# Kernel tuning notes

Hardware: AMD Instinct MI355X
Metric: run time of the kernel (lower is better)

## Reference

```python
import jax, jax.numpy as jnp
import numpy as np

EPS = 1e-7        # min norm to avoid div-by-zero
BALL_EPS = 1e-5   # Poincare-ball boundary clip


def _norm(x):
    return jnp.maximum(jnp.linalg.norm(x, axis=-1, keepdims=True), EPS)


def expmap0(u, c):
    sc = jnp.sqrt(c)
    n = _norm(u)
    return jnp.tanh(sc * n) * u / (sc * n)


def logmap0(p, c):
    sc = jnp.sqrt(c)
    n = _norm(p)
    return jnp.arctanh(jnp.minimum(sc * n, 1.0 - BALL_EPS)) * p / (sc * n)


def proj(x, c):
    # project onto the ball of radius (1-eps)/sqrt(c)
    n = _norm(x)
    maxn = (1.0 - BALL_EPS) / jnp.sqrt(c)
    return jnp.where(n > maxn, x * (maxn / n), x)


def mobius_matvec(W, x, c):
    # Mobius matrix-vector multiply on the Poincare ball
    sc = jnp.sqrt(c)
    xn = _norm(x)                       # [N,1]
    mx = x @ W                          # [N,D]
    mxn = _norm(mx)
    t = jnp.tanh((mxn / xn) * jnp.arctanh(jnp.minimum(sc * xn, 1.0 - BALL_EPS)))
    return t * mx / (sc * mxn)


def spmm(rows, cols, vals, x):
    # sparse(adj) @ x, adjacency in COO form
    return jax.ops.segment_sum(vals[:, None] * x[cols], rows, num_segments=x.shape[0])


def hgc_layer(x, rows, cols, vals, W, c, c_lin):
    t = logmap0(x, c)                               # to tangent space at origin
    h = proj(mobius_matvec(W, t, c_lin), c_lin)     # LinearHyperbolic (c=1.0, no activation)
    s = spmm(rows, cols, vals, h)                   # HyperbolicAggregation: adj @ h
    agg = proj(expmap0(s, c), c)
    a = jax.nn.relu(logmap0(agg, c))                # ActivationHyperbolic (relu, c_in=c_out=c)
    return proj(expmap0(a, c), c)


def setup_inputs() -> dict:
    key = jax.random.key(0)
    ks = jax.random.split(key, 7)
    N, D, E = 10000, 1433, 100000
    x = jax.random.normal(ks[0], (N, D), jnp.float32) * 0.1  # keep points off the boundary
    rows = jax.random.randint(ks[1], (E,), 0, N)
    cols = jax.random.randint(ks[2], (E,), 0, N)
    vals = jax.random.uniform(ks[3], (E,), jnp.float32) / 10.0  # ~normalized adjacency weights
    scale = 1.0 / np.sqrt(D)
    W0 = jax.random.normal(ks[4], (D, D), jnp.float32) * scale
    W1 = jax.random.normal(ks[5], (D, D), jnp.float32) * scale
    W2 = jax.random.normal(ks[6], (D, D), jnp.float32) * scale
    return {"x": x, "W0": W0, "W1": W1, "W2": W2, "vals": vals, "rows": rows, "cols": cols}


def reference(x, W0, W1, W2, vals, rows, cols):
    c = jnp.float32(0.4)       # c_map == c0 for every layer in the source
    c_lin = jnp.float32(1.0)   # LinearHyperbolic hard-coded c
    h = expmap0(x, c)
    for W in (W0, W1, W2):
        h = hgc_layer(h, rows, cols, vals, W, c, c_lin)
    return h
```

## Files before the change

kernel.cpp:

```cpp
#include <hip/hip_runtime.h>

typedef unsigned short u16;
typedef unsigned int   u32;

#define M_ROWS 10000
#define D_DIM  1433
#define KPAD   1536
#define MPAD   10240
#define N_EDGE 100000
#define HPAD   1440
#define HP32   720
#define NKT    24
#define EPS    1e-7f
#define BEPS   1e-5f
#define SC     0.6324555320336759f

typedef __bf16 bf16x8 __attribute__((ext_vector_type(8)));
typedef float  f32x4  __attribute__((ext_vector_type(4)));
typedef u32    u32x4  __attribute__((ext_vector_type(4)));

__device__ __forceinline__ u16 f2bf(float f) {
  union { float f; unsigned u; } v; v.f = f;
  unsigned r = v.u + 0x7FFFu + ((v.u >> 16) & 1u);
  return (u16)(r >> 16);
}
__device__ __forceinline__ u32 pack2bf(float lo, float hi) {
  return (u32)f2bf(lo) | ((u32)f2bf(hi) << 16);
}
__device__ __forceinline__ float bflo(u32 u) { return __uint_as_float(u << 16); }
__device__ __forceinline__ float bfhi(u32 u) { return __uint_as_float(u & 0xFFFF0000u); }

__device__ __forceinline__ float atanh_f(float y) {
  return 0.5f * logf((1.f + y) / (1.f - y));
}

__device__ __forceinline__ void gl_lds16(const u16* g, u16* l) {
  __builtin_amdgcn_global_load_lds((const __attribute__((address_space(1))) void*)(const void*)g,
                                   (__attribute__((address_space(3))) void*)(void*)l,
                                   16, 0, 0);
}

__global__ __launch_bounds__(512, 1) void gemm256(
    const u16* __restrict__ A,
    const u16* __restrict__ B,
    u16* __restrict__ C,
    float* __restrict__ nrm)
{
  __shared__ u16 lds[2][2][256 * 64];

  const int tid  = threadIdx.x;
  const int lane = tid & 63;
  const int w    = tid >> 6;
  const int wr   = w >> 2;
  const int wc   = w & 3;

  const int flat = blockIdx.x;
  const int wgid = (flat & 7) * 30 + (flat >> 3);
  const int gy = wgid % 6;
  const int gx = wgid / 6;
  const long arow0 = (long)gx * 256;
  const long brow0 = (long)gy * 256;

  f32x4 acc[8][4] = {};

  const int sr8 = lane >> 3;
  const int scb = ((lane & 7) << 4) ^ (sr8 << 4);

  auto STAGE = [&](int b, int kt) {
    const long k0 = (long)kt * 64 + (scb >> 1);
#pragma unroll
    for (int l = 0; l < 4; ++l) {
      const int r   = l * 64 + w * 8 + sr8;
      const int dst = l * 4096 + w * 512;
      gl_lds16(A + (arow0 + r) * KPAD + k0, &lds[b][0][dst]);
      gl_lds16(B + (brow0 + r) * KPAD + k0, &lds[b][1][dst]);
    }
  };

  STAGE(0, 0);
  __syncthreads();

  for (int kt = 0; kt < NKT; ++kt) {
    const int b = kt & 1;
    if (kt < NKT - 1) STAGE(b ^ 1, kt + 1);
#pragma unroll
    for (int ks = 0; ks < 2; ++ks) {
      bf16x8 af[8], bfr[4];
#pragma unroll
      for (int mi = 0; mi < 8; ++mi) {
        const int row = wr * 128 + mi * 16 + (lane & 15);
        const int kb  = (ks * 64 + ((lane >> 4) << 4)) ^ ((row & 7) << 4);
        af[mi] = *(const bf16x8*)&lds[b][0][row * 64 + (kb >> 1)];
      }
#pragma unroll
      for (int ni = 0; ni < 4; ++ni) {
        const int row = wc * 64 + ni * 16 + (lane & 15);
        const int kb  = (ks * 64 + ((lane >> 4) << 4)) ^ ((row & 7) << 4);
        bfr[ni] = *(const bf16x8*)&lds[b][1][row * 64 + (kb >> 1)];
      }
#pragma unroll
      for (int mi = 0; mi < 8; ++mi)
#pragma unroll
        for (int ni = 0; ni < 4; ++ni)
          acc[mi][ni] = __builtin_amdgcn_mfma_f32_16x16x32_bf16(af[mi], bfr[ni], acc[mi][ni], 0, 0, 0);
    }
    __syncthreads();
  }

  const int orw = (lane >> 4) * 4;
  const int ocl = lane & 15;

#pragma unroll
  for (int mi = 0; mi < 8; ++mi)
#pragma unroll
    for (int r = 0; r < 4; ++r) {
      float s = 0.f;
#pragma unroll
      for (int ni = 0; ni < 4; ++ni) {
        const long j = brow0 + wc * 64 + ni * 16 + ocl;
        const float v = acc[mi][ni][r];
        s += (j < D_DIM) ? v * v : 0.f;
      }
      s += __shfl_xor(s, 1, 64);
      s += __shfl_xor(s, 2, 64);
      s += __shfl_xor(s, 4, 64);
      s += __shfl_xor(s, 8, 64);
      if ((lane & 15) == 0)
        atomicAdd(&nrm[arow0 + wr * 128 + mi * 16 + orw + r], s);
    }

#pragma unroll
  for (int mi = 0; mi < 8; ++mi) {
    const long i0 = arow0 + wr * 128 + mi * 16 + orw;
    if (i0 >= M_ROWS) continue;
#pragma unroll
    for (int ni = 0; ni < 4; ++ni) {
      const long j = brow0 + wc * 64 + ni * 16 + ocl;
      if (j >= HPAD) continue;
#pragma unroll
      for (int r = 0; r < 4; ++r) {
        const long i = i0 + r;
        if (i < M_ROWS) C[i * HPAD + j] = (j < D_DIM) ? f2bf(acc[mi][ni][r]) : (u16)0;
      }
    }
  }
}

__device__ __forceinline__ float2 block_reduce2(float a, float b) {
  __shared__ float sa[4], sb[4];
#pragma unroll
  for (int off = 32; off > 0; off >>= 1) {
    a += __shfl_down(a, off, 64);
    b += __shfl_down(b, off, 64);
  }
  const int tid = threadIdx.x;
  if ((tid & 63) == 0) { sa[tid >> 6] = a; sb[tid >> 6] = b; }
  __syncthreads();
  const float ra = sa[0] + sa[1] + sa[2] + sa[3];
  const float rb = sb[0] + sb[1] + sb[2] + sb[3];
  __syncthreads();
  return make_float2(ra, rb);
}

__global__ __launch_bounds__(256) void pre_k(const float* __restrict__ x,
                                             u16* __restrict__ t,
                                             float* __restrict__ xn) {
  const long i = blockIdx.x;
  const int tid = threadIdx.x;
  u16* trow = t + i * KPAD;
  if (i >= M_ROWS) {
#pragma unroll
    for (int jj = 0; jj < 6; ++jj) { int j = tid + jj * 256; if (j < KPAD) trow[j] = 0; }
    return;
  }
  const float* xr = x + i * D_DIM;
  float v[6]; float s2 = 0.f;
#pragma unroll
  for (int jj = 0; jj < 6; ++jj) {
    int j = tid + jj * 256;
    v[jj] = (j < D_DIM) ? xr[j] : 0.f;
    s2 += v[jj] * v[jj];
  }
  s2 = block_reduce2(s2, 0.f).x;
  const float nx_t = sqrtf(s2);
  const float nx   = fmaxf(nx_t, EPS);
  const float al   = tanhf(SC * nx) / (SC * nx);
  const float n1   = fmaxf(al * nx_t, EPS);
  const float be   = atanh_f(fminf(SC * n1, 1.f - BEPS)) / (SC * n1);
  const float sca  = al * be;
  if (tid == 0) xn[i] = fmaxf(sca * nx_t, EPS);
#pragma unroll
  for (int jj = 0; jj < 6; ++jj) {
    int j = tid + jj * 256;
    if (j < KPAD) trow[j] = (j < D_DIM) ? f2bf(sca * v[jj]) : (u16)0;
  }
}

__global__ void zero_f(float* p, int n) {
  int i = blockIdx.x * 256 + threadIdx.x;
  if (i < n) p[i] = 0.f;
}

__global__ void fold_k(const int* __restrict__ ecol, const float* __restrict__ eval,
                       const float* __restrict__ nrm, const float* __restrict__ xn,
                       u32* __restrict__ pe, int E) {
  const int e = blockIdx.x * 256 + threadIdx.x;
  if (e >= E) return;
  const int c = ecol[e];
  const float realn = sqrtf(nrm[c]);
  const float mxn   = fmaxf(realn, EPS);
  const float xi    = xn[c];
  const float tf    = tanhf((mxn / xi) * atanh_f(fminf(xi, 1.f - BEPS)));
  float S = tf / mxn;
  const float hn = fmaxf(S * realn, EPS);
  const float maxn = 1.f - BEPS;
  if (hn > maxn) S *= maxn / hn;
  pe[e] = ((u32)c << 16) | (u32)f2bf(eval[e] * S);
}

__global__ __launch_bounds__(256) void spmm_post(const int* __restrict__ rp,
                                                 const u32* __restrict__ pe,
                                                 const u32* __restrict__ mxp,
                                                 u16* __restrict__ t,
                                                 float* __restrict__ xn,
                                                 float* __restrict__ out,
                                                 const int last) {
  const long r = blockIdx.x;
  const int tid = threadIdx.x;
  if (r >= M_ROWS) {
    if (!last && tid < 192) {
      u32* trow32 = (u32*)(t + r * KPAD);
#pragma unroll
      for (int k = 0; k < 4; ++k) trow32[4 * tid + k] = 0u;
    }
    return;
  }
  const bool act = tid < 180;
  const long boff = 4 * tid;
  float a[8] = {0.f, 0.f, 0.f, 0.f, 0.f, 0.f, 0.f, 0.f};
  const int e0 = rp[r], e1 = rp[r + 1];
  int e = e0;
  for (; e + 7 < e1; e += 8) {
    u32 pp[8];
#pragma unroll
    for (int j = 0; j < 8; ++j) pp[j] = pe[e + j];
    if (act) {
      u32x4 q[8];
#pragma unroll
      for (int j = 0; j < 8; ++j)
        q[j] = *(const u32x4*)&mxp[(long)(pp[j] >> 16) * HP32 + boff];
#pragma unroll
      for (int j = 0; j < 8; ++j) {
        const float w = bflo(pp[j]);
#pragma unroll
        for (int k = 0; k < 4; ++k) {
          a[2 * k]     += w * bflo(q[j][k]);
          a[2 * k + 1] += w * bfhi(q[j][k]);
        }
      }
    }
  }
  for (; e + 3 < e1; e += 4) {
    u32 pp[4];
#pragma unroll
    for (int j = 0; j < 4; ++j) pp[j] = pe[e + j];
    if (act) {
      u32x4 q[4];
#pragma unroll
      for (int j = 0; j < 4; ++j)
        q[j] = *(const u32x4*)&mxp[(long)(pp[j] >> 16) * HP32 + boff];
#pragma unroll
      for (int j = 0; j < 4; ++j) {
        const float w = bflo(pp[j]);
#pragma unroll
        for (int k = 0; k < 4; ++k) {
          a[2 * k]     += w * bflo(q[j][k]);
          a[2 * k + 1] += w * bfhi(q[j][k]);
        }
      }
    }
  }
  for (; e < e1; ++e) {
    const u32 p0 = pe[e];
    if (act) {
      const u32x4 q0 = *(const u32x4*)&mxp[(long)(p0 >> 16) * HP32 + boff];
      const float w0 = bflo(p0);
#pragma unroll
      for (int k = 0; k < 4; ++k) {
        a[2 * k]     += w0 * bflo(q0[k]);
        a[2 * k + 1] += w0 * bfhi(q0[k]);
      }
    }
  }
  float s2 = 0.f, s2p = 0.f;
#pragma unroll
  for (int k = 0; k < 8; ++k) {
    const int col = 8 * tid + k;
    const float v = (act && col < D_DIM) ? a[k] : 0.f;
    a[k] = v;
    s2 += v * v;
    const float p = fmaxf(v, 0.f);
    s2p += p * p;
  }
  const float2 red = block_reduce2(s2, s2p);
  const float ns_t  = sqrtf(red.x);
  const float nsp_t = sqrtf(red.y);
  const float maxn = (1.f - BEPS) / SC;
  const float ns = fmaxf(ns_t, EPS);
  const float al = tanhf(SC * ns) / (SC * ns);
  const float n1 = fmaxf(al * ns_t, EPS);
  const float be = (n1 > maxn) ? (maxn / n1) : 1.f;
  const float n2 = fmaxf(be * al * ns_t, EPS);
  const float lam = atanh_f(fminf(SC * n2, 1.f - BEPS)) / (SC * n2);
  const float g = lam * be * al;
  const float na_t = g * nsp_t;
  const float n3 = fmaxf(na_t, EPS);
  const float mu = tanhf(SC * n3) / (SC * n3);
  const float n4 = fmaxf(mu * na_t, EPS);
  const float nu = (n4 > maxn) ? (maxn / n4) : 1.f;
  const float T = nu * mu * g;
  if (last) {
    if (act) {
      float* orow = out + r * (long)D_DIM;
#pragma unroll
      for (int k = 0; k < 8; ++k) {
        const int col = 8 * tid + k;
        if (col < D_DIM) orow[col] = T * fmaxf(a[k], 0.f);
      }
    }
  } else {
    const float nh_t = T * nsp_t;
    const float n5 = fmaxf(nh_t, EPS);
    const float kap = atanh_f(fminf(SC * n5, 1.f - BEPS)) / (SC * n5);
    const float F = kap * T;
    if (tid == 0) xn[r] = fmaxf(F * nsp_t, EPS);
    u32* trow32 = (u32*)(t + r * KPAD);
    if (act) {
#pragma unroll
      for (int k = 0; k < 4; ++k)
        trow32[4 * tid + k] = pack2bf(F * fmaxf(a[2 * k], 0.f), F * fmaxf(a[2 * k + 1], 0.f));
    } else if (tid < 192) {
#pragma unroll
      for (int k = 0; k < 4; ++k) trow32[4 * tid + k] = 0u;
    }
  }
}

__global__ void wt_conv(const float* __restrict__ W, u16* __restrict__ Wt) {
  __shared__ float tile[32][33];
  const int kb = blockIdx.x * 32, nb = blockIdx.y * 32;
  const int tx = threadIdx.x, ty = threadIdx.y;
#pragma unroll
  for (int r = 0; r < 32; r += 8) {
    const int k = kb + ty + r, n = nb + tx;
    tile[ty + r][tx] = (k < D_DIM && n < D_DIM) ? W[(long)k * D_DIM + n] : 0.f;
  }
  __syncthreads();
#pragma unroll
  for (int r = 0; r < 32; r += 8) {
    const int n = nb + ty + r, k = kb + tx;
    if (n < KPAD && k < KPAD) Wt[(long)n * KPAD + k] = f2bf(tile[tx][ty + r]);
  }
}

__global__ void zero_int(int* p, int n) {
  int i = blockIdx.x * 256 + threadIdx.x;
  if (i < n) p[i] = 0;
}
__global__ void hist_k(const int* __restrict__ rows, int* __restrict__ counts, int E) {
  int e = blockIdx.x * 256 + threadIdx.x;
  if (e < E) atomicAdd(&counts[rows[e]], 1);
}
__global__ __launch_bounds__(1024) void scan_rp(const int* __restrict__ counts,
                                                int* __restrict__ rp, int n) {
  __shared__ int sd[1024];
  __shared__ int carry_s;
  const int tid = threadIdx.x;
  if (tid == 0) { carry_s = 0; rp[0] = 0; }
  __syncthreads();
  for (int base = 0; base < n; base += 1024) {
    const int i = base + tid;
    sd[tid] = (i < n) ? counts[i] : 0;
    __syncthreads();
    for (int off = 1; off < 1024; off <<= 1) {
      const int tv = (tid >= off) ? sd[tid - off] : 0;
      __syncthreads();
      sd[tid] += tv;
      __syncthreads();
    }
    const int carry = carry_s;
    if (i < n) rp[i + 1] = carry + sd[tid];
    __syncthreads();
    if (tid == 1023) carry_s = carry + sd[1023];
    __syncthreads();
  }
}
__global__ void scatter_k(const int* __restrict__ rows, const int* __restrict__ cols,
                          const float* __restrict__ vals, const int* __restrict__ rp,
                          int* __restrict__ cursor, int* __restrict__ ecol,
                          float* __restrict__ eval, int E) {
  int e = blockIdx.x * 256 + threadIdx.x;
  if (e < E) {
    const int r = rows[e];
    const int pos = rp[r] + atomicAdd(&cursor[r], 1);
    ecol[pos] = cols[e];
    eval[pos] = vals[e];
  }
}

extern "C" void kernel_launch(void* const* d_in, const int* in_sizes, int n_in,
                              void* d_out, int out_size, void* d_ws, size_t ws_size,
                              hipStream_t stream) {
  (void)in_sizes; (void)n_in; (void)out_size; (void)ws_size;
  const float* x    = (const float*)d_in[0];
  const float* W[3] = {(const float*)d_in[1], (const float*)d_in[2], (const float*)d_in[3]};
  const float* vals = (const float*)d_in[4];
  const int*   rows = (const int*)d_in[5];
  const int*   cols = (const int*)d_in[6];
  float* out = (float*)d_out;

  char* base = (char*)d_ws;
  size_t off = 0;
  auto take = [&](size_t bytes) {
    void* q = base + off;
    off = (off + bytes + 255) & ~(size_t)255;
    return q;
  };
  u16*   t    = (u16*)take((size_t)MPAD * KPAD * 2);
  u16*   Wt   = (u16*)take((size_t)KPAD * KPAD * 2);
  u16*   mx   = (u16*)take((size_t)M_ROWS * HPAD * 2);
  float* nrm3 = (float*)take((size_t)3 * MPAD * 4);
  float* xn   = (float*)take((size_t)M_ROWS * 4);
  int*   cnt  = (int*)take((size_t)M_ROWS * 2 * 4);
  int*   rp   = (int*)take((size_t)(M_ROWS + 1) * 4);
  int*   ecol = (int*)take((size_t)N_EDGE * 4);
  float* eval = (float*)take((size_t)N_EDGE * 4);
  u32*   pe   = (u32*)take((size_t)N_EDGE * 4);

  zero_int<<<(2 * M_ROWS + 255) / 256, 256, 0, stream>>>(cnt, 2 * M_ROWS);
  hist_k<<<(N_EDGE + 255) / 256, 256, 0, stream>>>(rows, cnt, N_EDGE);
  scan_rp<<<1, 1024, 0, stream>>>(cnt, rp, M_ROWS);
  scatter_k<<<(N_EDGE + 255) / 256, 256, 0, stream>>>(rows, cols, vals, rp,
                                                      cnt + M_ROWS, ecol, eval, N_EDGE);
  zero_f<<<(3 * MPAD + 255) / 256, 256, 0, stream>>>(nrm3, 3 * MPAD);

  pre_k<<<MPAD, 256, 0, stream>>>(x, t, xn);

  for (int L = 0; L < 3; ++L) {
    float* nrm = nrm3 + (size_t)L * MPAD;
    wt_conv<<<dim3(48, 48), dim3(32, 8), 0, stream>>>(W[L], Wt);
    gemm256<<<240, 512, 0, stream>>>(t, Wt, mx, nrm);
    fold_k<<<(N_EDGE + 255) / 256, 256, 0, stream>>>(ecol, eval, nrm, xn, pe, N_EDGE);
    spmm_post<<<MPAD, 256, 0, stream>>>(rp, pe, (const u32*)mx, t, xn, out, (L == 2) ? 1 : 0);
  }
}
```

Measured before the change: 374.0 us.

## Restructure GEMM main loop into ping-pong phases with prefetch-two staging

```diff
diff --git a/kernel.cpp b/kernel.cpp
--- a/kernel.cpp
+++ b/kernel.cpp
@@ -78,33 +78,54 @@
   };
 
   STAGE(0, 0);
-  __syncthreads();
+  STAGE(1, 1);
+  asm volatile("s_waitcnt vmcnt(8)" ::: "memory");
+  asm volatile("s_barrier" ::: "memory");
 
   for (int kt = 0; kt < NKT; ++kt) {
     const int b = kt & 1;
-    if (kt < NKT - 1) STAGE(b ^ 1, kt + 1);
-#pragma unroll
-    for (int ks = 0; ks < 2; ++ks) {
-      bf16x8 af[8], bfr[4];
-#pragma unroll
-      for (int mi = 0; mi < 8; ++mi) {
-        const int row = wr * 128 + mi * 16 + (lane & 15);
+    bf16x8 bfr[4];
+#pragma unroll
+    for (int p = 0; p < 4; ++p) {
+      const int ks = p >> 1;
+      const int mh = p & 1;
+      if (mh == 0) {
+#pragma unroll
+        for (int ni = 0; ni < 4; ++ni) {
+          const int row = wc * 64 + ni * 16 + (lane & 15);
+          const int kb  = (ks * 64 + ((lane >> 4) << 4)) ^ ((row & 7) << 4);
+          bfr[ni] = *(const bf16x8*)&lds[b][1][row * 64 + (kb >> 1)];
+        }
+      }
+      bf16x8 af[4];
+#pragma unroll
+      for (int ml = 0; ml < 4; ++ml) {
+        const int row = wr * 128 + (mh * 4 + ml) * 16 + (lane & 15);
         const int kb  = (ks * 64 + ((lane >> 4) << 4)) ^ ((row & 7) << 4);
-        af[mi] = *(const bf16x8*)&lds[b][0][row * 64 + (kb >> 1)];
-      }
-#pragma unroll
-      for (int ni = 0; ni < 4; ++ni) {
-        const int row = wc * 64 + ni * 16 + (lane & 15);
-        const int kb  = (ks * 64 + ((lane >> 4) << 4)) ^ ((row & 7) << 4);
-        bfr[ni] = *(const bf16x8*)&lds[b][1][row * 64 + (kb >> 1)];
-      }
-#pragma unroll
-      for (int mi = 0; mi < 8; ++mi)
+        af[ml] = *(const bf16x8*)&lds[b][0][row * 64 + (kb >> 1)];
+      }
+      asm volatile("s_barrier" ::: "memory");
+      asm volatile("s_waitcnt lgkmcnt(0)" ::: "memory");
+      __builtin_amdgcn_sched_barrier(0);
+      __builtin_amdgcn_s_setprio(1);
+#pragma unroll
+      for (int ml = 0; ml < 4; ++ml)
 #pragma unroll
         for (int ni = 0; ni < 4; ++ni)
-          acc[mi][ni] = __builtin_amdgcn_mfma_f32_16x16x32_bf16(af[mi], bfr[ni], acc[mi][ni], 0, 0, 0);
-    }
-    __syncthreads();
+          acc[mh * 4 + ml][ni] =
+              __builtin_amdgcn_mfma_f32_16x16x32_bf16(af[ml], bfr[ni], acc[mh * 4 + ml][ni], 0, 0, 0);
+      __builtin_amdgcn_s_setprio(0);
+      __builtin_amdgcn_sched_barrier(0);
+      asm volatile("s_barrier" ::: "memory");
+    }
+    if (kt + 2 < NKT) {
+      STAGE(b, kt + 2);
+      asm volatile("s_waitcnt vmcnt(8)" ::: "memory");
+      asm volatile("s_barrier" ::: "memory");
+    } else if (kt + 1 < NKT) {
+      asm volatile("s_waitcnt vmcnt(0)" ::: "memory");
+      asm volatile("s_barrier" ::: "memory");
+    }
   }
 
   const int orw = (lane >> 4) * 4;
```

Result: slower. 398.7 us (+6.6%).

## Split GEMM k-loop into two half-tiles interleaving prefetch with MFMA

Applied to the files above, without the earlier changes.

```diff
diff --git a/kernel.cpp b/kernel.cpp
--- a/kernel.cpp
+++ b/kernel.cpp
@@ -66,45 +66,92 @@
   const int sr8 = lane >> 3;
   const int scb = ((lane & 7) << 4) ^ (sr8 << 4);
 
-  auto STAGE = [&](int b, int kt) {
+  auto STG_B = [&](int b, int kt) {
     const long k0 = (long)kt * 64 + (scb >> 1);
 #pragma unroll
     for (int l = 0; l < 4; ++l) {
       const int r   = l * 64 + w * 8 + sr8;
       const int dst = l * 4096 + w * 512;
+      gl_lds16(B + (brow0 + r) * KPAD + k0, &lds[b][1][dst]);
+    }
+  };
+  auto STG_A = [&](int b, int kt, int sel) {
+    const long k0 = (long)kt * 64 + (scb >> 1);
+#pragma unroll
+    for (int li = 0; li < 2; ++li) {
+      const int l   = sel + 2 * li;
+      const int r   = l * 64 + w * 8 + sr8;
+      const int dst = l * 4096 + w * 512;
       gl_lds16(A + (arow0 + r) * KPAD + k0, &lds[b][0][dst]);
-      gl_lds16(B + (brow0 + r) * KPAD + k0, &lds[b][1][dst]);
     }
   };
 
-  STAGE(0, 0);
-  __syncthreads();
+  STG_B(0, 0); STG_A(0, 0, 0); STG_A(0, 0, 1);
+  asm volatile("s_waitcnt vmcnt(0)" ::: "memory");
+  __builtin_amdgcn_s_barrier();
 
   for (int kt = 0; kt < NKT; ++kt) {
     const int b = kt & 1;
-    if (kt < NKT - 1) STAGE(b ^ 1, kt + 1);
-#pragma unroll
-    for (int ks = 0; ks < 2; ++ks) {
-      bf16x8 af[8], bfr[4];
-#pragma unroll
-      for (int mi = 0; mi < 8; ++mi) {
-        const int row = wr * 128 + mi * 16 + (lane & 15);
-        const int kb  = (ks * 64 + ((lane >> 4) << 4)) ^ ((row & 7) << 4);
-        af[mi] = *(const bf16x8*)&lds[b][0][row * 64 + (kb >> 1)];
-      }
-#pragma unroll
-      for (int ni = 0; ni < 4; ++ni) {
-        const int row = wc * 64 + ni * 16 + (lane & 15);
-        const int kb  = (ks * 64 + ((lane >> 4) << 4)) ^ ((row & 7) << 4);
-        bfr[ni] = *(const bf16x8*)&lds[b][1][row * 64 + (kb >> 1)];
-      }
-#pragma unroll
-      for (int mi = 0; mi < 8; ++mi)
-#pragma unroll
-        for (int ni = 0; ni < 4; ++ni)
-          acc[mi][ni] = __builtin_amdgcn_mfma_f32_16x16x32_bf16(af[mi], bfr[ni], acc[mi][ni], 0, 0, 0);
-    }
-    __syncthreads();
+    const bool pf = (kt + 1 < NKT);
+
+    bf16x8 b0[4], b1[4], a0[4], a1[4];
+#pragma unroll
+    for (int ni = 0; ni < 4; ++ni) {
+      const int row = wc * 64 + ni * 16 + (lane & 15);
+      const int kb0 = (((lane >> 4) << 4)) ^ ((row & 7) << 4);
+      const int kb1 = (64 + ((lane >> 4) << 4)) ^ ((row & 7) << 4);
+      b0[ni] = *(const bf16x8*)&lds[b][1][row * 64 + (kb0 >> 1)];
+      b1[ni] = *(const bf16x8*)&lds[b][1][row * 64 + (kb1 >> 1)];
+    }
+#pragma unroll
+    for (int ml = 0; ml < 4; ++ml) {
+      const int row = wr * 128 + ml * 16 + (lane & 15);
+      const int kb0 = (((lane >> 4) << 4)) ^ ((row & 7) << 4);
+      const int kb1 = (64 + ((lane >> 4) << 4)) ^ ((row & 7) << 4);
+      a0[ml] = *(const bf16x8*)&lds[b][0][row * 64 + (kb0 >> 1)];
+      a1[ml] = *(const bf16x8*)&lds[b][0][row * 64 + (kb1 >> 1)];
+    }
+    if (pf) { STG_B(b ^ 1, kt + 1); STG_A(b ^ 1, kt + 1, 0); }
+    __builtin_amdgcn_s_setprio(1);
+#pragma unroll
+    for (int ml = 0; ml < 4; ++ml)
+#pragma unroll
+      for (int ni = 0; ni < 4; ++ni)
+        acc[ml][ni] = __builtin_amdgcn_mfma_f32_16x16x32_bf16(a0[ml], b0[ni], acc[ml][ni], 0, 0, 0);
+#pragma unroll
+    for (int ml = 0; ml < 4; ++ml)
+#pragma unroll
+      for (int ni = 0; ni < 4; ++ni)
+        acc[ml][ni] = __builtin_amdgcn_mfma_f32_16x16x32_bf16(a1[ml], b1[ni], acc[ml][ni], 0, 0, 0);
+    __builtin_amdgcn_s_setprio(0);
+    if (pf) asm volatile("s_waitcnt vmcnt(6)" ::: "memory");
+    else    asm volatile("s_waitcnt vmcnt(0)" ::: "memory");
+    __builtin_amdgcn_s_barrier();
+
+    bf16x8 c0[4], c1[4];
+#pragma unroll
+    for (int ml = 0; ml < 4; ++ml) {
+      const int row = wr * 128 + (4 + ml) * 16 + (lane & 15);
+      const int kb0 = (((lane >> 4) << 4)) ^ ((row & 7) << 4);
+      const int kb1 = (64 + ((lane >> 4) << 4)) ^ ((row & 7) << 4);
+      c0[ml] = *(const bf16x8*)&lds[b][0][row * 64 + (kb0 >> 1)];
+      c1[ml] = *(const bf16x8*)&lds[b][0][row * 64 + (kb1 >> 1)];
+    }
+    if (pf) STG_A(b ^ 1, kt + 1, 1);
+    __builtin_amdgcn_s_setprio(1);
+#pragma unroll
+    for (int ml = 0; ml < 4; ++ml)
+#pragma unroll
+      for (int ni = 0; ni < 4; ++ni)
+        acc[4 + ml][ni] = __builtin_amdgcn_mfma_f32_16x16x32_bf16(c0[ml], b0[ni], acc[4 + ml][ni], 0, 0, 0);
+#pragma unroll
+    for (int ml = 0; ml < 4; ++ml)
+#pragma unroll
+      for (int ni = 0; ni < 4; ++ni)
+        acc[4 + ml][ni] = __builtin_amdgcn_mfma_f32_16x16x32_bf16(c1[ml], b1[ni], acc[4 + ml][ni], 0, 0, 0);
+    __builtin_amdgcn_s_setprio(0);
+    if (pf) asm volatile("s_waitcnt vmcnt(2)" ::: "memory");
+    __builtin_amdgcn_s_barrier();
   }
 
   const int orw = (lane >> 4) * 4;
```

Result: no change. 370.1 us (-1.0%).
